# Kernel tuning notes

Measured on AMD Instinct MI355X. Metric: run time of the kernel, lower is better.

## Reference

```python
import jax, jax.numpy as jnp
import numpy as np

NUM_BANDS = 12
D_MODEL = 128
NUM_HEADS = 2
HEAD_DIM = D_MODEL // NUM_HEADS


def setup_inputs() -> dict:
    key = jax.random.key(0)
    ks = jax.random.split(key, 12)
    d, B = D_MODEL, NUM_BANDS
    return {
        "x": jax.random.normal(ks[0], (4, 128, 128, B), dtype=jnp.float32),
        "w_embed": jax.random.normal(ks[1], (d,), dtype=jnp.float32) * 0.05,
        "b_embed": jax.random.normal(ks[2], (d,), dtype=jnp.float32) * 0.05,
        "band_pos": jax.random.normal(ks[3], (B, d), dtype=jnp.float32) * 0.02,
        "Wq": jax.random.normal(ks[4], (d, d), dtype=jnp.float32) * (1.0 / np.sqrt(d)),
        "bq": jax.random.normal(ks[5], (d,), dtype=jnp.float32) * 0.02,
        "Wk": jax.random.normal(ks[6], (d, d), dtype=jnp.float32) * (1.0 / np.sqrt(d)),
        "bk": jax.random.normal(ks[7], (d,), dtype=jnp.float32) * 0.02,
        "Wv": jax.random.normal(ks[8], (d, d), dtype=jnp.float32) * (1.0 / np.sqrt(d)),
        "bv": jax.random.normal(ks[9], (d,), dtype=jnp.float32) * 0.02,
        # out_proj is zero-init in the module; use tiny random values so the
        # output is numerically non-trivial for kernel correctness checks.
        "Wo": jax.random.normal(ks[10], (1, d), dtype=jnp.float32) * 0.02,
        "bo": jax.random.normal(ks[11], (1,), dtype=jnp.float32) * 0.02,
    }


def reference(x, w_embed, b_embed, band_pos, Wq, bq, Wk, bk, Wv, bv, Wo, bo):
    shape = x.shape
    x_flat = x.reshape(-1, NUM_BANDS)  # [N, B]
    N = x_flat.shape[0]
    H, hd = NUM_HEADS, HEAD_DIM
    # band_embed (Linear(1, d)) + band identity embedding -> tokens [N, B, d]
    tokens = x_flat[..., None] * w_embed + b_embed + band_pos
    # QKV projections, split heads
    Q = (tokens @ Wq.T + bq).reshape(N, NUM_BANDS, H, hd)
    K = (tokens @ Wk.T + bk).reshape(N, NUM_BANDS, H, hd)
    V = (tokens @ Wv.T + bv).reshape(N, NUM_BANDS, H, hd)
    scale = 1.0 / np.sqrt(hd).astype(np.float32)
    attn = jnp.einsum("nqhd,nkhd->nhqk", Q, K) * scale  # [N, H, B, B]
    attn = jax.nn.softmax(attn, axis=-1)
    out = jnp.einsum("nhqk,nkhd->nqhd", attn, V).reshape(N, NUM_BANDS, D_MODEL)
    delta = (out @ Wo.T + bo)[..., 0]  # out_proj -> [N, B]
    return (x_flat + delta).reshape(shape)
```

## Files before the change

kernel.cpp:

```cpp
#include <hip/hip_runtime.h>

#define D_MODEL 128
#define NBANDS 12
#define NHEADS 2
#define HDIM 64
#define NCONSTS 364

__global__ void spectral_inter_kernel(
    const float* __restrict__ w_embed, const float* __restrict__ b_embed,
    const float* __restrict__ band_pos,
    const float* __restrict__ Wq, const float* __restrict__ bq,
    const float* __restrict__ Wk, const float* __restrict__ bk,
    const float* __restrict__ Wv, const float* __restrict__ bv,
    float* __restrict__ inter)
{
    const int m = blockIdx.x / 13;
    const int c = blockIdx.x % 13;
    const int t = threadIdx.x;
    const float* M    = (m == 0) ? Wq : (m == 1) ? Wk : Wv;
    const float* bias = (m == 0) ? bq : (m == 1) ? bk : bv;
    const float* row  = M + t * D_MODEL;
    float s = 0.f;
    if (c == 0) {
        #pragma unroll 8
        for (int j = 0; j < D_MODEL; ++j) s = fmaf(row[j], w_embed[j], s);
    } else {
        const float* bpr = band_pos + (c - 1) * D_MODEL;
        #pragma unroll 8
        for (int j = 0; j < D_MODEL; ++j) s = fmaf(row[j], b_embed[j] + bpr[j], s);
        s += bias[t];
    }
    inter[(m * 13 + c) * D_MODEL + t] = s;
}

__global__ __launch_bounds__(256) void spectral_main_kernel(
    const float* __restrict__ x, const float* __restrict__ Wo,
    const float* __restrict__ bo, const float* __restrict__ inter,
    float* __restrict__ out, int n_tokens)
{
    __shared__ float sc[NCONSTS];
    const int t = threadIdx.x;
    const float* qv = inter;
    const float* kv = inter + 13 * D_MODEL;
    const float* vv = inter + 26 * D_MODEL;

    for (int idx = t; idx < NCONSTS; idx += 256) {
        float s = 0.f;
        if (idx < 2) {
            int h = idx;
            for (int d = 0; d < HDIM; ++d) s = fmaf(qv[h*HDIM+d], kv[h*HDIM+d], s);
            s *= 0.125f;
        } else if (idx < 4) {
            int h = idx - 2;
            for (int d = 0; d < HDIM; ++d) s = fmaf(vv[h*HDIM+d], Wo[h*HDIM+d], s);
        } else if (idx < 28) {
            int i = idx - 4, h = i / NBANDS, k = i % NBANDS;
            const float* kc = kv + (1 + k) * D_MODEL;
            for (int d = 0; d < HDIM; ++d) s = fmaf(qv[h*HDIM+d], kc[h*HDIM+d], s);
            s *= 0.125f;
        } else if (idx < 52) {
            int i = idx - 28, h = i / NBANDS, q = i % NBANDS;
            const float* qc = qv + (1 + q) * D_MODEL;
            for (int d = 0; d < HDIM; ++d) s = fmaf(qc[h*HDIM+d], kv[h*HDIM+d], s);
            s *= 0.125f;
        } else if (idx < 76) {
            int i = idx - 52, h = i / NBANDS, k = i % NBANDS;
            const float* vc = vv + (1 + k) * D_MODEL;
            for (int d = 0; d < HDIM; ++d) s = fmaf(vc[h*HDIM+d], Wo[h*HDIM+d], s);
        } else {
            int i = idx - 76, h = i / (NBANDS*NBANDS);
            int q = (i / NBANDS) % NBANDS, k = i % NBANDS;
            const float* qc = qv + (1 + q) * D_MODEL;
            const float* kc = kv + (1 + k) * D_MODEL;
            for (int d = 0; d < HDIM; ++d) s = fmaf(qc[h*HDIM+d], kc[h*HDIM+d], s);
            s *= 0.125f;
        }
        sc[idx] = s;
    }
    __syncthreads();

    const int n = blockIdx.x * 256 + t;
    if (n >= n_tokens) return;

    const float4* xin = reinterpret_cast<const float4*>(x + (size_t)n * NBANDS);
    float4 p0 = xin[0], p1 = xin[1], p2 = xin[2];
    float xb[NBANDS] = {p0.x,p0.y,p0.z,p0.w, p1.x,p1.y,p1.z,p1.w, p2.x,p2.y,p2.z,p2.w};

    float acc[NBANDS];
    const float bo_v = bo[0];
    #pragma unroll
    for (int q = 0; q < NBANDS; ++q) acc[q] = bo_v;

    #pragma unroll
    for (int h = 0; h < NHEADS; ++h) {
        const float a = sc[h];
        const float e = sc[2 + h];
        const float* u = &sc[4  + h * NBANDS];
        const float* v = &sc[28 + h * NBANDS];
        const float* g = &sc[52 + h * NBANDS];
        const float* w = &sc[76 + h * NBANDS * NBANDS];
        for (int q = 0; q < NBANDS; ++q) {
            const float xq   = xb[q];
            const float coef = fmaf(a, xq, v[q]);
            const float* wq  = w + q * NBANDS;
            float s[NBANDS];
            float m = -1e30f;
            #pragma unroll
            for (int k = 0; k < NBANDS; ++k) {
                float sv = fmaf(coef, xb[k], fmaf(u[k], xq, wq[k]));
                s[k] = sv;
                m = fmaxf(m, sv);
            }
            float den = 0.f, num = 0.f;
            #pragma unroll
            for (int k = 0; k < NBANDS; ++k) {
                float p = __expf(s[k] - m);
                den += p;
                num  = fmaf(p, fmaf(e, xb[k], g[k]), num);
            }
            acc[q] = fmaf(num, __builtin_amdgcn_rcpf(den), acc[q]);
        }
    }

    float4 o0 = make_float4(p0.x + acc[0], p0.y + acc[1], p0.z + acc[2],  p0.w + acc[3]);
    float4 o1 = make_float4(p1.x + acc[4], p1.y + acc[5], p1.z + acc[6],  p1.w + acc[7]);
    float4 o2 = make_float4(p2.x + acc[8], p2.y + acc[9], p2.z + acc[10], p2.w + acc[11]);
    float4* op = reinterpret_cast<float4*>(out + (size_t)n * NBANDS);
    op[0] = o0; op[1] = o1; op[2] = o2;
}

extern "C" void kernel_launch(void* const* d_in, const int* in_sizes, int n_in,
                              void* d_out, int out_size, void* d_ws, size_t ws_size,
                              hipStream_t stream)
{
    const float* x  = (const float*)d_in[0];
    const float* we = (const float*)d_in[1];
    const float* be = (const float*)d_in[2];
    const float* bp = (const float*)d_in[3];
    const float* Wq = (const float*)d_in[4];
    const float* bq = (const float*)d_in[5];
    const float* Wk = (const float*)d_in[6];
    const float* bk = (const float*)d_in[7];
    const float* Wv = (const float*)d_in[8];
    const float* bv = (const float*)d_in[9];
    const float* Wo = (const float*)d_in[10];
    const float* bo = (const float*)d_in[11];
    float* out   = (float*)d_out;
    float* inter = (float*)d_ws;

    const int n_tokens = in_sizes[0] / NBANDS;

    hipLaunchKernelGGL(spectral_inter_kernel, dim3(39), dim3(128), 0, stream,
                       we, be, bp, Wq, bq, Wk, bk, Wv, bv, inter);
    hipLaunchKernelGGL(spectral_main_kernel,
                       dim3((n_tokens + 255) / 256), dim3(256), 0, stream,
                       x, Wo, bo, inter, out, n_tokens);
}
```

Measured before the change: 96.21 us.

## Hoist per-block constant computation into separate kernel and parallelize per band-query

Computes the 364 attention constants once in a dedicated single-block kernel that stages the intermediate projections in shared memory, so each main-kernel block only copies them instead of recomputing dot products from global memory. The main kernel now assigns one thread per (token, query band) instead of one per token, giving twelve times more threads and a smaller per-thread register footprint. In exchange, each thread redundantly reloads the token's full 12-band row, stores become scalar, and an extra kernel launch is added to the serial chain.

```diff
diff --git a/kernel.cpp b/kernel.cpp
--- a/kernel.cpp
+++ b/kernel.cpp
@@ -5,6 +5,7 @@
 #define NHEADS 2
 #define HDIM 64
 #define NCONSTS 364
+#define NINTER (39 * D_MODEL)
 
 __global__ void spectral_inter_kernel(
     const float* __restrict__ w_embed, const float* __restrict__ b_embed,
@@ -33,100 +34,111 @@
     inter[(m * 13 + c) * D_MODEL + t] = s;
 }
 
+__global__ __launch_bounds__(384) void spectral_consts_kernel(
+    const float* __restrict__ inter, const float* __restrict__ Wo,
+    float* __restrict__ consts)
+{
+    __shared__ float si[NINTER];
+    __shared__ float swo[D_MODEL];
+    const int t = threadIdx.x;
+    for (int i = t; i < NINTER; i += 384) si[i] = inter[i];
+    for (int i = t; i < D_MODEL; i += 384) swo[i] = Wo[i];
+    __syncthreads();
+
+    const int idx = t;
+    if (idx >= NCONSTS) return;
+    const float* qv = si;
+    const float* kv = si + 13 * D_MODEL;
+    const float* vv = si + 26 * D_MODEL;
+
+    float s = 0.f;
+    if (idx < 2) {
+        int h = idx;
+        #pragma unroll 8
+        for (int d = 0; d < HDIM; ++d) s = fmaf(qv[h*HDIM+d], kv[h*HDIM+d], s);
+        s *= 0.125f;
+    } else if (idx < 4) {
+        int h = idx - 2;
+        #pragma unroll 8
+        for (int d = 0; d < HDIM; ++d) s = fmaf(vv[h*HDIM+d], swo[h*HDIM+d], s);
+    } else if (idx < 28) {
+        int i = idx - 4, h = i / NBANDS, k = i % NBANDS;
+        const float* kc = kv + (1 + k) * D_MODEL;
+        #pragma unroll 8
+        for (int d = 0; d < HDIM; ++d) s = fmaf(qv[h*HDIM+d], kc[h*HDIM+d], s);
+        s *= 0.125f;
+    } else if (idx < 52) {
+        int i = idx - 28, h = i / NBANDS, q = i % NBANDS;
+        const float* qc = qv + (1 + q) * D_MODEL;
+        #pragma unroll 8
+        for (int d = 0; d < HDIM; ++d) s = fmaf(qc[h*HDIM+d], kv[h*HDIM+d], s);
+        s *= 0.125f;
+    } else if (idx < 76) {
+        int i = idx - 52, h = i / NBANDS, k = i % NBANDS;
+        const float* vc = vv + (1 + k) * D_MODEL;
+        #pragma unroll 8
+        for (int d = 0; d < HDIM; ++d) s = fmaf(vc[h*HDIM+d], swo[h*HDIM+d], s);
+    } else {
+        int i = idx - 76, h = i / (NBANDS*NBANDS);
+        int q = (i / NBANDS) % NBANDS, k = i % NBANDS;
+        const float* qc = qv + (1 + q) * D_MODEL;
+        const float* kc = kv + (1 + k) * D_MODEL;
+        #pragma unroll 8
+        for (int d = 0; d < HDIM; ++d) s = fmaf(qc[h*HDIM+d], kc[h*HDIM+d], s);
+        s *= 0.125f;
+    }
+    consts[idx] = s;
+}
+
 __global__ __launch_bounds__(256) void spectral_main_kernel(
-    const float* __restrict__ x, const float* __restrict__ Wo,
-    const float* __restrict__ bo, const float* __restrict__ inter,
-    float* __restrict__ out, int n_tokens)
+    const float* __restrict__ x, const float* __restrict__ bo,
+    const float* __restrict__ consts, float* __restrict__ out, int n_total)
 {
     __shared__ float sc[NCONSTS];
     const int t = threadIdx.x;
-    const float* qv = inter;
-    const float* kv = inter + 13 * D_MODEL;
-    const float* vv = inter + 26 * D_MODEL;
-
-    for (int idx = t; idx < NCONSTS; idx += 256) {
-        float s = 0.f;
-        if (idx < 2) {
-            int h = idx;
-            for (int d = 0; d < HDIM; ++d) s = fmaf(qv[h*HDIM+d], kv[h*HDIM+d], s);
-            s *= 0.125f;
-        } else if (idx < 4) {
-            int h = idx - 2;
-            for (int d = 0; d < HDIM; ++d) s = fmaf(vv[h*HDIM+d], Wo[h*HDIM+d], s);
-        } else if (idx < 28) {
-            int i = idx - 4, h = i / NBANDS, k = i % NBANDS;
-            const float* kc = kv + (1 + k) * D_MODEL;
-            for (int d = 0; d < HDIM; ++d) s = fmaf(qv[h*HDIM+d], kc[h*HDIM+d], s);
-            s *= 0.125f;
-        } else if (idx < 52) {
-            int i = idx - 28, h = i / NBANDS, q = i % NBANDS;
-            const float* qc = qv + (1 + q) * D_MODEL;
-            for (int d = 0; d < HDIM; ++d) s = fmaf(qc[h*HDIM+d], kv[h*HDIM+d], s);
-            s *= 0.125f;
-        } else if (idx < 76) {
-            int i = idx - 52, h = i / NBANDS, k = i % NBANDS;
-            const float* vc = vv + (1 + k) * D_MODEL;
-            for (int d = 0; d < HDIM; ++d) s = fmaf(vc[h*HDIM+d], Wo[h*HDIM+d], s);
-        } else {
-            int i = idx - 76, h = i / (NBANDS*NBANDS);
-            int q = (i / NBANDS) % NBANDS, k = i % NBANDS;
-            const float* qc = qv + (1 + q) * D_MODEL;
-            const float* kc = kv + (1 + k) * D_MODEL;
-            for (int d = 0; d < HDIM; ++d) s = fmaf(qc[h*HDIM+d], kc[h*HDIM+d], s);
-            s *= 0.125f;
-        }
-        sc[idx] = s;
-    }
+    for (int i = t; i < NCONSTS; i += 256) sc[i] = consts[i];
     __syncthreads();
 
-    const int n = blockIdx.x * 256 + t;
-    if (n >= n_tokens) return;
+    const int tid = blockIdx.x * 256 + t;
+    if (tid >= n_total) return;
+
+    const unsigned n = (unsigned)tid / 12u;
+    const int q = tid - (int)n * 12;
 
     const float4* xin = reinterpret_cast<const float4*>(x + (size_t)n * NBANDS);
     float4 p0 = xin[0], p1 = xin[1], p2 = xin[2];
     float xb[NBANDS] = {p0.x,p0.y,p0.z,p0.w, p1.x,p1.y,p1.z,p1.w, p2.x,p2.y,p2.z,p2.w};
+    const float xq = x[tid];
 
-    float acc[NBANDS];
-    const float bo_v = bo[0];
-    #pragma unroll
-    for (int q = 0; q < NBANDS; ++q) acc[q] = bo_v;
-
+    float acc = bo[0];
     #pragma unroll
     for (int h = 0; h < NHEADS; ++h) {
         const float a = sc[h];
         const float e = sc[2 + h];
-        const float* u = &sc[4  + h * NBANDS];
-        const float* v = &sc[28 + h * NBANDS];
-        const float* g = &sc[52 + h * NBANDS];
-        const float* w = &sc[76 + h * NBANDS * NBANDS];
-        for (int q = 0; q < NBANDS; ++q) {
-            const float xq   = xb[q];
-            const float coef = fmaf(a, xq, v[q]);
-            const float* wq  = w + q * NBANDS;
-            float s[NBANDS];
-            float m = -1e30f;
-            #pragma unroll
-            for (int k = 0; k < NBANDS; ++k) {
-                float sv = fmaf(coef, xb[k], fmaf(u[k], xq, wq[k]));
-                s[k] = sv;
-                m = fmaxf(m, sv);
-            }
-            float den = 0.f, num = 0.f;
-            #pragma unroll
-            for (int k = 0; k < NBANDS; ++k) {
-                float p = __expf(s[k] - m);
-                den += p;
-                num  = fmaf(p, fmaf(e, xb[k], g[k]), num);
-            }
-            acc[q] = fmaf(num, __builtin_amdgcn_rcpf(den), acc[q]);
+        const float* u  = &sc[4  + h * NBANDS];
+        const float vq  = sc[28 + h * NBANDS + q];
+        const float* g  = &sc[52 + h * NBANDS];
+        const float* wq = &sc[76 + h * NBANDS * NBANDS + q * NBANDS];
+        const float coef = fmaf(a, xq, vq);
+        float s[NBANDS];
+        float m = -1e30f;
+        #pragma unroll
+        for (int k = 0; k < NBANDS; ++k) {
+            float sv = fmaf(coef, xb[k], fmaf(u[k], xq, wq[k]));
+            s[k] = sv;
+            m = fmaxf(m, sv);
         }
+        float den = 0.f, num = 0.f;
+        #pragma unroll
+        for (int k = 0; k < NBANDS; ++k) {
+            float p = __expf(s[k] - m);
+            den += p;
+            num  = fmaf(p, fmaf(e, xb[k], g[k]), num);
+        }
+        acc = fmaf(num, __builtin_amdgcn_rcpf(den), acc);
     }
 
-    float4 o0 = make_float4(p0.x + acc[0], p0.y + acc[1], p0.z + acc[2],  p0.w + acc[3]);
-    float4 o1 = make_float4(p1.x + acc[4], p1.y + acc[5], p1.z + acc[6],  p1.w + acc[7]);
-    float4 o2 = make_float4(p2.x + acc[8], p2.y + acc[9], p2.z + acc[10], p2.w + acc[11]);
-    float4* op = reinterpret_cast<float4*>(out + (size_t)n * NBANDS);
-    op[0] = o0; op[1] = o1; op[2] = o2;
+    out[tid] = xq + acc;
 }
 
 extern "C" void kernel_launch(void* const* d_in, const int* in_sizes, int n_in,
@@ -145,14 +157,17 @@
     const float* bv = (const float*)d_in[9];
     const float* Wo = (const float*)d_in[10];
     const float* bo = (const float*)d_in[11];
-    float* out   = (float*)d_out;
-    float* inter = (float*)d_ws;
+    float* out    = (float*)d_out;
+    float* inter  = (float*)d_ws;
+    float* consts = (float*)d_ws + NINTER;
 
-    const int n_tokens = in_sizes[0] / NBANDS;
+    const int n_total = in_sizes[0];
 
     hipLaunchKernelGGL(spectral_inter_kernel, dim3(39), dim3(128), 0, stream,
                        we, be, bp, Wq, bq, Wk, bk, Wv, bv, inter);
+    hipLaunchKernelGGL(spectral_consts_kernel, dim3(1), dim3(384), 0, stream,
+                       inter, Wo, consts);
     hipLaunchKernelGGL(spectral_main_kernel,
-                       dim3((n_tokens + 255) / 256), dim3(256), 0, stream,
-                       x, Wo, bo, inter, out, n_tokens);
+                       dim3((n_total + 255) / 256), dim3(256), 0, stream,
+                       x, bo, consts, out, n_total);
 }
```

After: 96.09 us. Within noise of the previous version (-0.1%).
